# Optimization experiments

Hardware: AMD Instinct MI355X
Metric: run time of the kernel (lower is better)

## Reference

```python
import jax, jax.numpy as jnp
import numpy as np

B, N, H, F = 4, 4096, 128, 64
ADJ_DENSITY = 0.01


def setup_inputs() -> dict:
    key = jax.random.key(0)
    k1, k2, k3, k4, k5 = jax.random.split(key, 5)
    x = jax.random.normal(k1, (B, N, H), dtype=jnp.float32)
    w_scale = jnp.float32(1.0 / np.sqrt(H))  # ~ nn.Linear init scale
    Wq = jax.random.normal(k2, (H, F), dtype=jnp.float32) * w_scale
    Wk = jax.random.normal(k3, (H, F), dtype=jnp.float32) * w_scale
    Wv = jax.random.normal(k4, (H, F), dtype=jnp.float32) * w_scale
    # Sparse binary adjacency with self-loops (every row has >=1 neighbor,
    # so no all--inf softmax rows).
    adj = (jax.random.uniform(k5, (N, N)) < ADJ_DENSITY).astype(jnp.float32)
    diag = jnp.arange(N)
    adj = adj.at[diag, diag].set(1.0)
    return {"x": x, "Wq": Wq, "Wk": Wk, "Wv": Wv, "adj": adj}


def reference(x, Wq, Wk, Wv, adj):
    # x: (B,N,H); Wq/Wk/Wv: (H,F); adj: (N,N) binary, broadcast over batch.
    q = x @ Wq  # (B,N,F)
    k = x @ Wk  # (B,N,F)
    v = x @ Wv  # (B,N,F)
    scale = jnp.float32(F) ** -0.5  # k.shape[-1] ** -0.5
    scores = jnp.einsum("bnf,bmf->bnm", q, k) * scale  # (B,N,N)
    scores = jnp.where(adj[None] == 0, -jnp.inf, scores)
    # softmax over neighbors, then the module adds the adjacency back (wei + adj)
    wei = jax.nn.softmax(scores, axis=-1) + adj[None]  # (B,N,N)
    # dropout is identity in eval/deterministic reference
    out = jnp.einsum("bnm,bmf->bnf", wei, v)  # (B,N,F)
    return out
```

## Files before the change

kernel.cpp:

```cpp
#include <hip/hip_runtime.h>
#include <math.h>

#define Bb 4
#define Nn 4096
#define Hh 128
#define Ff 64
#define CAP 128

#define CSR_GRID 256
#define QKV_GRID 256

typedef __attribute__((ext_vector_type(8))) short bf16x8;
typedef __attribute__((ext_vector_type(4))) float f32x4;

__device__ __forceinline__ unsigned short f2bf(float f) {
  unsigned int u = __float_as_uint(f);
  u += 0x7fffu + ((u >> 16) & 1u);
  return (unsigned short)(u >> 16);
}
__device__ __forceinline__ float bf2f(unsigned short h) {
  return __uint_as_float(((unsigned int)h) << 16);
}

__global__ __launch_bounds__(256) void prep_kernel(
    const float* __restrict__ x,
    const float* __restrict__ Wq,
    const float* __restrict__ Wk,
    const float* __restrict__ Wv,
    const float* __restrict__ adj,
    float* __restrict__ q,
    unsigned short* __restrict__ kb,
    unsigned short* __restrict__ vb,
    unsigned short* __restrict__ g_nbr, int* __restrict__ g_cnt) {
  __shared__ short xs[64 * 128];

  const int tid = threadIdx.x;
  const int w = tid >> 6;
  const int lane = tid & 63;

  if (blockIdx.x >= CSR_GRID) {
    const int row0 = (int)(blockIdx.x - CSR_GRID) * 64;
    const int half = lane >> 4;
    const int l16 = lane & 15;

    const float4* xg = (const float4*)(x + (size_t)row0 * Hh);
#pragma unroll
    for (int j = 0; j < 8; ++j) {
      const int idx = tid + 256 * j;
      const int row = idx >> 5;
      const int c4 = idx & 31;
      const float4 xv = xg[idx];
      uint2 p;
      p.x = (unsigned)f2bf(xv.x) | ((unsigned)f2bf(xv.y) << 16);
      p.y = (unsigned)f2bf(xv.z) | ((unsigned)f2bf(xv.w) << 16);
      const int addr = (row * 256 + c4 * 8) ^ ((row & 7) << 4);
      *(uint2*)((char*)xs + addr) = p;
    }

    bf16x8 bfr[3][4];
#pragma unroll
    for (int nt = 0; nt < 3; ++nt) {
      const int n0g = w * 48 + nt * 16;
      const float* Wm = (n0g < 64) ? Wq : (n0g < 128) ? Wk : Wv;
      const int c0 = n0g & 63;
#pragma unroll
      for (int ks = 0; ks < 4; ++ks) {
        bf16x8 f;
#pragma unroll
        for (int j = 0; j < 8; ++j) {
          const int kr = ks * 32 + half * 8 + j;
          f[j] = (short)f2bf(Wm[kr * Ff + c0 + l16]);
        }
        bfr[nt][ks] = f;
      }
    }
    __syncthreads();

    f32x4 acc[4][3];
#pragma unroll
    for (int mt = 0; mt < 4; ++mt)
#pragma unroll
      for (int nt = 0; nt < 3; ++nt)
#pragma unroll
        for (int r = 0; r < 4; ++r) acc[mt][nt][r] = 0.f;

#pragma unroll
    for (int mt = 0; mt < 4; ++mt) {
      const int arow = mt * 16 + l16;
      const int abase = arow * 256;
      const int aswz = (arow & 7) << 4;
#pragma unroll
      for (int ks = 0; ks < 4; ++ks) {
        const int addr = (abase + ks * 64 + half * 16) ^ aswz;
        const bf16x8 a = *(const bf16x8*)((const char*)xs + addr);
#pragma unroll
        for (int nt = 0; nt < 3; ++nt) {
          acc[mt][nt] = __builtin_amdgcn_mfma_f32_16x16x32_bf16(
              a, bfr[nt][ks], acc[mt][nt], 0, 0, 0);
        }
      }
    }

#pragma unroll
    for (int mt = 0; mt < 4; ++mt) {
#pragma unroll
      for (int nt = 0; nt < 3; ++nt) {
        const int n0g = w * 48 + nt * 16;
        const int col = (n0g & 63) + l16;
#pragma unroll
        for (int r = 0; r < 4; ++r) {
          const size_t rowg = (size_t)row0 + mt * 16 + half * 4 + r;
          const float val = acc[mt][nt][r];
          if (n0g < 64)
            q[rowg * Ff + col] = val;
          else if (n0g < 128)
            kb[rowg * Ff + col] = f2bf(val);
          else
            vb[rowg * Ff + col] = f2bf(val);
        }
      }
    }
  } else {
    const int nbase = (int)blockIdx.x * 16 + w * 4;
    const unsigned long long ltmask =
        (lane == 0) ? 0ull : (~0ull >> (64 - lane));

    for (int rr = 0; rr < 4; ++rr) {
      const int n = nbase + rr;
      const float* arow = adj + (size_t)n * Nn;
      unsigned short* nrow = g_nbr + (size_t)n * CAP;

      float4 a4[16];
#pragma unroll
      for (int c = 0; c < 16; ++c) a4[c] = ((const float4*)arow)[c * 64 + lane];

      int off = 0;
#pragma unroll
      for (int c = 0; c < 16; ++c) {
#pragma unroll
        for (int comp = 0; comp < 4; ++comp) {
          const float val = comp == 0 ? a4[c].x
                          : comp == 1 ? a4[c].y
                          : comp == 2 ? a4[c].z
                                      : a4[c].w;
          const bool nz = (val != 0.f);
          const unsigned long long mm = __ballot(nz);
          if (nz) {
            const int pos = off + (int)__popcll(mm & ltmask);
            if (pos < CAP)
              nrow[pos] = (unsigned short)(c * 256 + 4 * lane + comp);
          }
          off += (int)__popcll(mm);
        }
      }
      if (lane == 0) g_cnt[n] = off < CAP ? off : CAP;
    }
  }
}

__global__ __launch_bounds__(256) void attn_kernel(
    const unsigned short* __restrict__ g_nbr,
    const int* __restrict__ g_cnt,
    const float* __restrict__ q,
    const unsigned short* __restrict__ kb,
    const unsigned short* __restrict__ vb,
    float* __restrict__ out) {
  __shared__ __align__(8) unsigned short nbr[CAP];
  __shared__ float qs[4][64];
  __shared__ float ps[4][64];

  const int n = blockIdx.x;
  const int tid = threadIdx.x;
  const int w = tid >> 6;
  const int lane = tid & 63;

  qs[w][lane] = q[((size_t)w * Nn + n) * Ff + lane];
  if (w == 0) {
    ((ushort2*)nbr)[lane] = ((const ushort2*)(g_nbr + (size_t)n * CAP))[lane];
  }
  const int tot = g_cnt[n];
  __syncthreads();

  const int b = w;
  const unsigned short* kbb = kb + (size_t)b * Nn * Ff;
  const unsigned short* vbb = vb + (size_t)b * Nn * Ff;

  const int g = lane >> 2;
  const int sl = lane & 3;

  float4 q0a = *(const float4*)&qs[b][8 * sl];
  float4 q0b = *(const float4*)&qs[b][8 * sl + 4];
  float4 q1a = *(const float4*)&qs[b][32 + 8 * sl];
  float4 q1b = *(const float4*)&qs[b][32 + 8 * sl + 4];

  float M = -INFINITY, L = 0.f, acc = 0.f, vsum = 0.f;

  const int ntiles = (tot + 63) >> 6;
  for (int t = 0; t < ntiles; ++t) {
    const int tbase = t << 6;

    float s0, s1, s2, s3;
#define BPAIR(u, qlo, qhi, a)                                   \
    {                                                           \
      const float flo = __uint_as_float((u) << 16);             \
      const float fhi = __uint_as_float((u) & 0xffff0000u);     \
      a = fmaf(qlo, flo, a);                                    \
      a = fmaf(qhi, fhi, a);                                    \
    }
#define DOT_ROW(i, sdst)                                                  \
    {                                                                     \
      const int idx = tbase + g + 16 * (i);                               \
      const bool valid = idx < tot;                                       \
      const int m = valid ? (int)nbr[idx] : 0;                            \
      const char* krow = (const char*)(kbb + (size_t)m * Ff);             \
      const uint4 k0 = *(const uint4*)(krow + 16 * sl);                   \
      const uint4 k1 = *(const uint4*)(krow + 64 + 16 * sl);              \
      float a = 0.f;                                                      \
      BPAIR(k0.x, q0a.x, q0a.y, a)                                        \
      BPAIR(k0.y, q0a.z, q0a.w, a)                                        \
      BPAIR(k0.z, q0b.x, q0b.y, a)                                        \
      BPAIR(k0.w, q0b.z, q0b.w, a)                                        \
      BPAIR(k1.x, q1a.x, q1a.y, a)                                        \
      BPAIR(k1.y, q1a.z, q1a.w, a)                                        \
      BPAIR(k1.z, q1b.x, q1b.y, a)                                        \
      BPAIR(k1.w, q1b.z, q1b.w, a)                                        \
      a += __shfl_xor(a, 1, 64);                                          \
      a += __shfl_xor(a, 2, 64);                                          \
      sdst = valid ? a * 0.125f : -INFINITY;                              \
    }
    DOT_ROW(0, s0)
    DOT_ROW(1, s1)
    DOT_ROW(2, s2)
    DOT_ROW(3, s3)
#undef DOT_ROW
#undef BPAIR

    float lm = fmaxf(fmaxf(s0, s1), fmaxf(s2, s3));
#pragma unroll
    for (int o = 32; o; o >>= 1) lm = fmaxf(lm, __shfl_xor(lm, o, 64));
    const float newM = fmaxf(M, lm);

    const float p0 = (s0 == -INFINITY) ? 0.f : __expf(s0 - newM);
    const float p1 = (s1 == -INFINITY) ? 0.f : __expf(s1 - newM);
    const float p2 = (s2 == -INFINITY) ? 0.f : __expf(s2 - newM);
    const float p3 = (s3 == -INFINITY) ? 0.f : __expf(s3 - newM);

    float psum = ((p0 + p1) + (p2 + p3));
#pragma unroll
    for (int o = 32; o >= 4; o >>= 1) psum += __shfl_xor(psum, o, 64);

    const float corr = __expf(M - newM);
    L = L * corr + psum;
    acc *= corr;
    M = newM;

    const float pw = sl == 0 ? p0 : sl == 1 ? p1 : sl == 2 ? p2 : p3;
    ps[w][g + 16 * sl] = pw;

    const int jmax = min(64, tot - tbase);
#pragma unroll 4
    for (int j = 0; j < jmax; ++j) {
      const int m = nbr[tbase + j];
      const float vf = bf2f(vbb[(size_t)m * Ff + lane]);
      acc = fmaf(ps[w][j], vf, acc);
      vsum += vf;
    }
  }

  out[((size_t)b * Nn + n) * Ff + lane] = acc / L + vsum;
}

extern "C" void kernel_launch(void* const* d_in, const int* in_sizes, int n_in,
                              void* d_out, int out_size, void* d_ws, size_t ws_size,
                              hipStream_t stream) {
  const float* x = (const float*)d_in[0];
  const float* Wq = (const float*)d_in[1];
  const float* Wk = (const float*)d_in[2];
  const float* Wv = (const float*)d_in[3];
  const float* adj = (const float*)d_in[4];
  float* out = (float*)d_out;

  char* ws = (char*)d_ws;
  const size_t rows = (size_t)Bb * Nn;
  float* q = (float*)ws;
  unsigned short* kb = (unsigned short*)(ws + rows * Ff * 4);
  unsigned short* vb = (unsigned short*)(ws + rows * Ff * 4 + rows * Ff * 2);
  unsigned short* g_nbr = (unsigned short*)(ws + rows * Ff * 8);
  int* g_cnt = (int*)(ws + rows * Ff * 8 + (size_t)Nn * CAP * 2);

  prep_kernel<<<dim3(CSR_GRID + QKV_GRID), dim3(256), 0, stream>>>(
      x, Wq, Wk, Wv, adj, q, kb, vb, g_nbr, g_cnt);
  attn_kernel<<<dim3(Nn), dim3(256), 0, stream>>>(g_nbr, g_cnt, q, kb, vb, out);
}
```

Measured before the change: 47.38 us.

## Split fused prep kernel into separate QKV and CSR kernels with LDS staging

```diff
diff --git a/kernel.cpp b/kernel.cpp
--- a/kernel.cpp
+++ b/kernel.cpp
@@ -7,9 +7,6 @@
 #define Ff 64
 #define CAP 128
 
-#define CSR_GRID 256
-#define QKV_GRID 256
-
 typedef __attribute__((ext_vector_type(8))) short bf16x8;
 typedef __attribute__((ext_vector_type(4))) float f32x4;
 
@@ -22,140 +19,146 @@
   return __uint_as_float(((unsigned int)h) << 16);
 }
 
-__global__ __launch_bounds__(256) void prep_kernel(
+__global__ __launch_bounds__(256) void qkv_kernel(
     const float* __restrict__ x,
     const float* __restrict__ Wq,
     const float* __restrict__ Wk,
     const float* __restrict__ Wv,
-    const float* __restrict__ adj,
     float* __restrict__ q,
     unsigned short* __restrict__ kb,
-    unsigned short* __restrict__ vb,
-    unsigned short* __restrict__ g_nbr, int* __restrict__ g_cnt) {
+    unsigned short* __restrict__ vb) {
   __shared__ short xs[64 * 128];
 
   const int tid = threadIdx.x;
   const int w = tid >> 6;
   const int lane = tid & 63;
 
-  if (blockIdx.x >= CSR_GRID) {
-    const int row0 = (int)(blockIdx.x - CSR_GRID) * 64;
-    const int half = lane >> 4;
-    const int l16 = lane & 15;
-
-    const float4* xg = (const float4*)(x + (size_t)row0 * Hh);
-#pragma unroll
-    for (int j = 0; j < 8; ++j) {
-      const int idx = tid + 256 * j;
-      const int row = idx >> 5;
-      const int c4 = idx & 31;
-      const float4 xv = xg[idx];
-      uint2 p;
-      p.x = (unsigned)f2bf(xv.x) | ((unsigned)f2bf(xv.y) << 16);
-      p.y = (unsigned)f2bf(xv.z) | ((unsigned)f2bf(xv.w) << 16);
-      const int addr = (row * 256 + c4 * 8) ^ ((row & 7) << 4);
-      *(uint2*)((char*)xs + addr) = p;
-    }
-
-    bf16x8 bfr[3][4];
+  const int row0 = (int)blockIdx.x * 64;
+  const int half = lane >> 4;
+  const int l16 = lane & 15;
+
+  const float4* xg = (const float4*)(x + (size_t)row0 * Hh);
+#pragma unroll
+  for (int j = 0; j < 8; ++j) {
+    const int idx = tid + 256 * j;
+    const int row = idx >> 5;
+    const int c4 = idx & 31;
+    const float4 xv = xg[idx];
+    uint2 p;
+    p.x = (unsigned)f2bf(xv.x) | ((unsigned)f2bf(xv.y) << 16);
+    p.y = (unsigned)f2bf(xv.z) | ((unsigned)f2bf(xv.w) << 16);
+    const int addr = (row * 256 + c4 * 8) ^ ((row & 7) << 4);
+    *(uint2*)((char*)xs + addr) = p;
+  }
+
+  bf16x8 bfr[3][4];
+#pragma unroll
+  for (int nt = 0; nt < 3; ++nt) {
+    const int n0g = w * 48 + nt * 16;
+    const float* Wm = (n0g < 64) ? Wq : (n0g < 128) ? Wk : Wv;
+    const int c0 = n0g & 63;
+#pragma unroll
+    for (int ks = 0; ks < 4; ++ks) {
+      bf16x8 f;
+#pragma unroll
+      for (int j = 0; j < 8; ++j) {
+        const int kr = ks * 32 + half * 8 + j;
+        f[j] = (short)f2bf(Wm[kr * Ff + c0 + l16]);
+      }
+      bfr[nt][ks] = f;
+    }
+  }
+  __syncthreads();
+
+  f32x4 acc[4][3];
+#pragma unroll
+  for (int mt = 0; mt < 4; ++mt)
+#pragma unroll
+    for (int nt = 0; nt < 3; ++nt)
+#pragma unroll
+      for (int r = 0; r < 4; ++r) acc[mt][nt][r] = 0.f;
+
+#pragma unroll
+  for (int mt = 0; mt < 4; ++mt) {
+    const int arow = mt * 16 + l16;
+    const int abase = arow * 256;
+    const int aswz = (arow & 7) << 4;
+#pragma unroll
+    for (int ks = 0; ks < 4; ++ks) {
+      const int addr = (abase + ks * 64 + half * 16) ^ aswz;
+      const bf16x8 a = *(const bf16x8*)((const char*)xs + addr);
+#pragma unroll
+      for (int nt = 0; nt < 3; ++nt) {
+        acc[mt][nt] = __builtin_amdgcn_mfma_f32_16x16x32_bf16(
+            a, bfr[nt][ks], acc[mt][nt], 0, 0, 0);
+      }
+    }
+  }
+
+#pragma unroll
+  for (int mt = 0; mt < 4; ++mt) {
 #pragma unroll
     for (int nt = 0; nt < 3; ++nt) {
       const int n0g = w * 48 + nt * 16;
-      const float* Wm = (n0g < 64) ? Wq : (n0g < 128) ? Wk : Wv;
-      const int c0 = n0g & 63;
-#pragma unroll
-      for (int ks = 0; ks < 4; ++ks) {
-        bf16x8 f;
-#pragma unroll
-        for (int j = 0; j < 8; ++j) {
-          const int kr = ks * 32 + half * 8 + j;
-          f[j] = (short)f2bf(Wm[kr * Ff + c0 + l16]);
-        }
-        bfr[nt][ks] = f;
-      }
-    }
-    __syncthreads();
-
-    f32x4 acc[4][3];
-#pragma unroll
-    for (int mt = 0; mt < 4; ++mt)
-#pragma unroll
-      for (int nt = 0; nt < 3; ++nt)
-#pragma unroll
-        for (int r = 0; r < 4; ++r) acc[mt][nt][r] = 0.f;
-
-#pragma unroll
-    for (int mt = 0; mt < 4; ++mt) {
-      const int arow = mt * 16 + l16;
-      const int abase = arow * 256;
-      const int aswz = (arow & 7) << 4;
-#pragma unroll
-      for (int ks = 0; ks < 4; ++ks) {
-        const int addr = (abase + ks * 64 + half * 16) ^ aswz;
-        const bf16x8 a = *(const bf16x8*)((const char*)xs + addr);
-#pragma unroll
-        for (int nt = 0; nt < 3; ++nt) {
-          acc[mt][nt] = __builtin_amdgcn_mfma_f32_16x16x32_bf16(
-              a, bfr[nt][ks], acc[mt][nt], 0, 0, 0);
-        }
-      }
-    }
-
-#pragma unroll
-    for (int mt = 0; mt < 4; ++mt) {
-#pragma unroll
-      for (int nt = 0; nt < 3; ++nt) {
-        const int n0g = w * 48 + nt * 16;
-        const int col = (n0g & 63) + l16;
-#pragma unroll
-        for (int r = 0; r < 4; ++r) {
-          const size_t rowg = (size_t)row0 + mt * 16 + half * 4 + r;
-          const float val = acc[mt][nt][r];
-          if (n0g < 64)
-            q[rowg * Ff + col] = val;
-          else if (n0g < 128)
-            kb[rowg * Ff + col] = f2bf(val);
-          else
-            vb[rowg * Ff + col] = f2bf(val);
-        }
-      }
-    }
-  } else {
-    const int nbase = (int)blockIdx.x * 16 + w * 4;
-    const unsigned long long ltmask =
-        (lane == 0) ? 0ull : (~0ull >> (64 - lane));
-
-    for (int rr = 0; rr < 4; ++rr) {
-      const int n = nbase + rr;
-      const float* arow = adj + (size_t)n * Nn;
-      unsigned short* nrow = g_nbr + (size_t)n * CAP;
-
-      float4 a4[16];
-#pragma unroll
-      for (int c = 0; c < 16; ++c) a4[c] = ((const float4*)arow)[c * 64 + lane];
-
-      int off = 0;
-#pragma unroll
-      for (int c = 0; c < 16; ++c) {
-#pragma unroll
-        for (int comp = 0; comp < 4; ++comp) {
-          const float val = comp == 0 ? a4[c].x
-                          : comp == 1 ? a4[c].y
-                          : comp == 2 ? a4[c].z
-                                      : a4[c].w;
-          const bool nz = (val != 0.f);
-          const unsigned long long mm = __ballot(nz);
-          if (nz) {
-            const int pos = off + (int)__popcll(mm & ltmask);
-            if (pos < CAP)
-              nrow[pos] = (unsigned short)(c * 256 + 4 * lane + comp);
-          }
-          off += (int)__popcll(mm);
-        }
-      }
-      if (lane == 0) g_cnt[n] = off < CAP ? off : CAP;
-    }
-  }
+      const int col = (n0g & 63) + l16;
+#pragma unroll
+      for (int r = 0; r < 4; ++r) {
+        const size_t rowg = (size_t)row0 + mt * 16 + half * 4 + r;
+        const float val = acc[mt][nt][r];
+        if (n0g < 64)
+          q[rowg * Ff + col] = val;
+        else if (n0g < 128)
+          kb[rowg * Ff + col] = f2bf(val);
+        else
+          vb[rowg * Ff + col] = f2bf(val);
+      }
+    }
+  }
+}
+
+__global__ __launch_bounds__(256) void csr_kernel(
+    const float* __restrict__ adj,
+    unsigned short* __restrict__ g_nbr,
+    int* __restrict__ g_cnt) {
+  __shared__ __align__(8) unsigned short stg[4][CAP];
+
+  const int tid = threadIdx.x;
+  const int w = tid >> 6;
+  const int lane = tid & 63;
+
+  const int n = (int)blockIdx.x * 4 + w;
+  const float* arow = adj + (size_t)n * Nn;
+
+  ((ushort2*)stg[w])[lane] = make_ushort2(0, 0);
+
+  float4 a4[16];
+#pragma unroll
+  for (int c = 0; c < 16; ++c) a4[c] = ((const float4*)arow)[c * 64 + lane];
+
+  const unsigned long long ltmask =
+      (lane == 0) ? 0ull : (~0ull >> (64 - lane));
+  int off = 0;
+#pragma unroll
+  for (int c = 0; c < 16; ++c) {
+#pragma unroll
+    for (int comp = 0; comp < 4; ++comp) {
+      const float val = comp == 0 ? a4[c].x
+                      : comp == 1 ? a4[c].y
+                      : comp == 2 ? a4[c].z
+                                  : a4[c].w;
+      const bool nz = (val != 0.f);
+      const unsigned long long mm = __ballot(nz);
+      if (nz) {
+        const int pos = off + (int)__popcll(mm & ltmask);
+        if (pos < CAP)
+          stg[w][pos] = (unsigned short)(c * 256 + 4 * lane + comp);
+      }
+      off += (int)__popcll(mm);
+    }
+  }
+
+  if (lane == 0) g_cnt[n] = off < CAP ? off : CAP;
+  ((ushort2*)(g_nbr + (size_t)n * CAP))[lane] = ((const ushort2*)stg[w])[lane];
 }
 
 __global__ __launch_bounds__(256) void attn_kernel(
@@ -288,7 +291,7 @@
   unsigned short* g_nbr = (unsigned short*)(ws + rows * Ff * 8);
   int* g_cnt = (int*)(ws + rows * Ff * 8 + (size_t)Nn * CAP * 2);
 
-  prep_kernel<<<dim3(CSR_GRID + QKV_GRID), dim3(256), 0, stream>>>(
-      x, Wq, Wk, Wv, adj, q, kb, vb, g_nbr, g_cnt);
+  qkv_kernel<<<dim3(256), dim3(256), 0, stream>>>(x, Wq, Wk, Wv, q, kb, vb);
+  csr_kernel<<<dim3(Nn / 4), dim3(256), 0, stream>>>(adj, g_nbr, g_cnt);
   attn_kernel<<<dim3(Nn), dim3(256), 0, stream>>>(g_nbr, g_cnt, q, kb, vb, out);
 }
```

New measurement: 55.23 us. +16.6%, slower.
